# Optimization experiments

Hardware: AMD Instinct MI355X
Metric: run time of the kernel (lower is better)

Reference implementation:

```python
import jax, jax.numpy as jnp
import numpy as np


def setup_inputs() -> dict:
    key = jax.random.key(0)
    kx, kw = jax.random.split(key)
    x = jax.random.normal(kx, (8192, 4096), dtype=jnp.float32)
    # weights initialized ~ N(0, 0.1) as in RandomNormal(stddev=0.1)
    w = jax.random.normal(kw, (4096, 4096), dtype=jnp.float32) * 0.1
    return {"x": x, "w": w}


def reference(x, w):
    # BinaryDense: sign-binarize both activations and weights, then matmul.
    x_bin = jnp.sign(x)  # [N, d_in], values in {-1, 0, +1}
    w_bin = jnp.sign(w)  # [d_in, units]
    return jnp.matmul(x_bin, w_bin)  # [N, units]
```

## Files before the change

### kernel.cpp

```cpp
#include <hip/hip_runtime.h>


#define M_DIM 8192
#define K_DIM 4096
#define N_DIM 4096
#define KB2   (K_DIM / 2)

typedef int   v4i  __attribute__((ext_vector_type(4)));
typedef int   v8i  __attribute__((ext_vector_type(8)));
typedef float v16f __attribute__((ext_vector_type(16)));

typedef __attribute__((address_space(3))) void lds_void_t;
typedef __attribute__((address_space(1))) void g_void_t;

__device__ __forceinline__ unsigned int nib4(float x) {
    return x > 0.0f ? 0x2u : (x < 0.0f ? 0xAu : 0x0u);
}

__global__ __launch_bounds__(256) void pack_x4(const float* __restrict__ in,
                                               unsigned short* __restrict__ out) {
    size_t t = (size_t)blockIdx.x * 256 + threadIdx.x;
    float4 f = ((const float4*)in)[t];
    unsigned int v = nib4(f.x) | (nib4(f.y) << 4) | (nib4(f.z) << 8) | (nib4(f.w) << 12);
    out[t] = (unsigned short)v;
}

__global__ __launch_bounds__(256) void pack_w4(const float* __restrict__ w,
                                               unsigned char* __restrict__ wT) {
    __shared__ unsigned char sT[64][132];
    const int t  = threadIdx.x;
    const int n0 = blockIdx.x * 128;
    const int k0 = blockIdx.y * 64;

    const int cq = t & 31;
    const int r0 = t >> 5;
#pragma unroll
    for (int p = 0; p < 8; ++p) {
        int r = r0 + 8 * p;
        float4 f = *(const float4*)(w + (size_t)(k0 + r) * N_DIM + n0 + cq * 4);
        uchar4 c;
        c.x = (unsigned char)nib4(f.x);
        c.y = (unsigned char)nib4(f.y);
        c.z = (unsigned char)nib4(f.z);
        c.w = (unsigned char)nib4(f.w);
        *(uchar4*)(&sT[r][cq * 4]) = c;
    }
    __syncthreads();

    const int n  = t >> 1;
    const int kq = t & 1;
    union { unsigned char b[16]; int4 v; } u;
#pragma unroll
    for (int j = 0; j < 16; ++j) {
        unsigned lo = sT[kq * 32 + 2 * j][n];
        unsigned hi = sT[kq * 32 + 2 * j + 1][n];
        u.b[j] = (unsigned char)(lo | (hi << 4));
    }
    *(int4*)(wT + (size_t)(n0 + n) * KB2 + (size_t)blockIdx.y * 32 + kq * 16) = u.v;
}

__device__ __forceinline__ v8i widen(v4i x) {
    v8i r;
    r[0] = x[0]; r[1] = x[1]; r[2] = x[2]; r[3] = x[3];
    r[4] = 0; r[5] = 0; r[6] = 0; r[7] = 0;
    return r;
}

__global__ __launch_bounds__(256) void bgemm_fp4(const unsigned char* __restrict__ A,
                                                 const unsigned char* __restrict__ B,
                                                 float* __restrict__ C) {
    __shared__ unsigned char sA[128 * 64];
    __shared__ unsigned char sB[128 * 64];

    const int tid  = threadIdx.x;
    const int lane = tid & 63;
    const int wave = tid >> 6;
    const int wm   = wave >> 1;
    const int wn   = wave & 1;
    const int l31  = lane & 31;
    const int lhi  = lane >> 5;

    const int m0 = blockIdx.y * 128;
    const int n0 = blockIdx.x * 128;

    v16f acc[2][2] = {};

    const unsigned char* gA[2];
    const unsigned char* gB[2];
    int ldsOff[2];
#pragma unroll
    for (int i = 0; i < 2; ++i) {
        int g  = tid + i * 256;
        int m  = g >> 2;
        int kc = (g & 3) ^ ((m >> 1) & 3);
        gA[i] = A + (size_t)(m0 + m) * KB2 + kc * 16;
        gB[i] = B + (size_t)(n0 + m) * KB2 + kc * 16;
        ldsOff[i] = g * 16;
    }

    int offA[2][2], offB[2][2];
#pragma unroll
    for (int ks = 0; ks < 2; ++ks) {
#pragma unroll
        for (int tmn = 0; tmn < 2; ++tmn) {
            int mloc = wm * 64 + tmn * 32 + l31;
            int nloc = wn * 64 + tmn * 32 + l31;
            int kcm  = (ks * 2 + lhi) ^ ((mloc >> 1) & 3);
            int kcn  = (ks * 2 + lhi) ^ ((nloc >> 1) & 3);
            offA[ks][tmn] = mloc * 64 + kcm * 16;
            offB[ks][tmn] = nloc * 64 + kcn * 16;
        }
    }

    for (int kt = 0; kt < K_DIM / 128; ++kt) {
        const size_t koff = (size_t)kt * 64;
#pragma unroll
        for (int i = 0; i < 2; ++i) {
            __builtin_amdgcn_global_load_lds((g_void_t*)(gA[i] + koff),
                                             (lds_void_t*)(sA + ldsOff[i]), 16, 0, 0);
            __builtin_amdgcn_global_load_lds((g_void_t*)(gB[i] + koff),
                                             (lds_void_t*)(sB + ldsOff[i]), 16, 0, 0);
        }
        __syncthreads();

#pragma unroll
        for (int ks = 0; ks < 2; ++ks) {
            v4i a4[2], b4[2];
#pragma unroll
            for (int tm = 0; tm < 2; ++tm) a4[tm] = *(const v4i*)(sA + offA[ks][tm]);
#pragma unroll
            for (int tn = 0; tn < 2; ++tn) b4[tn] = *(const v4i*)(sB + offB[ks][tn]);
#pragma unroll
            for (int tm = 0; tm < 2; ++tm)
#pragma unroll
                for (int tn = 0; tn < 2; ++tn)
                    acc[tm][tn] = __builtin_amdgcn_mfma_scale_f32_32x32x64_f8f6f4(
                        widen(a4[tm]), widen(b4[tn]), acc[tm][tn],
                        4, 4,
                        0, 0x7F7F7F7F,
                        0, 0x7F7F7F7F);
        }
        __syncthreads();
    }

#pragma unroll
    for (int tm = 0; tm < 2; ++tm) {
#pragma unroll
        for (int tn = 0; tn < 2; ++tn) {
            const int col  = n0 + wn * 64 + tn * 32 + l31;
            const int rowb = m0 + wm * 64 + tm * 32 + 4 * lhi;
#pragma unroll
            for (int r = 0; r < 16; ++r) {
                int row = rowb + (r & 3) + 8 * (r >> 2);
                C[(size_t)row * N_DIM + col] = acc[tm][tn][r];
            }
        }
    }
}

extern "C" void kernel_launch(void* const* d_in, const int* in_sizes, int n_in,
                              void* d_out, int out_size, void* d_ws, size_t ws_size,
                              hipStream_t stream) {
    const float* x = (const float*)d_in[0];
    const float* w = (const float*)d_in[1];
    float* out = (float*)d_out;

    unsigned char* xq = (unsigned char*)d_ws;
    unsigned char* wq = xq + (size_t)M_DIM * KB2;

    pack_x4<<<dim3(M_DIM * K_DIM / 4 / 256), dim3(256), 0, stream>>>(x, (unsigned short*)xq);
    pack_w4<<<dim3(N_DIM / 128, K_DIM / 64), dim3(256), 0, stream>>>(w, wq);
    bgemm_fp4<<<dim3(N_DIM / 128, M_DIM / 128), dim3(256), 0, stream>>>(xq, wq, out);
}
```

Measured before the change: 328.0 us.

## Double-buffer GEMM LDS via register prefetch, fuse pack kernels, nontemporal stores

Replaces direct global-to-LDS loads with register-staged prefetch into a double-buffered LDS tile, so the next K tile is loaded while MFMAs run on the current one and only one barrier per iteration remains. Merges the two packing kernels into one launch to save launch overhead and let them run concurrently. Output stores become nontemporal to avoid polluting cache. Costs more LDS and registers per block, which may reduce occupancy.

```diff
diff --git a/kernel.cpp b/kernel.cpp
--- a/kernel.cpp
+++ b/kernel.cpp
@@ -5,32 +5,34 @@
 #define K_DIM 4096
 #define N_DIM 4096
 #define KB2   (K_DIM / 2)
+#define NK    (K_DIM / 128)
+#define BUFB  (128 * 64)
 
 typedef int   v4i  __attribute__((ext_vector_type(4)));
 typedef int   v8i  __attribute__((ext_vector_type(8)));
 typedef float v16f __attribute__((ext_vector_type(16)));
 
-typedef __attribute__((address_space(3))) void lds_void_t;
-typedef __attribute__((address_space(1))) void g_void_t;
-
 __device__ __forceinline__ unsigned int nib4(float x) {
     return x > 0.0f ? 0x2u : (x < 0.0f ? 0xAu : 0x0u);
 }
 
-__global__ __launch_bounds__(256) void pack_x4(const float* __restrict__ in,
-                                               unsigned short* __restrict__ out) {
-    size_t t = (size_t)blockIdx.x * 256 + threadIdx.x;
-    float4 f = ((const float4*)in)[t];
-    unsigned int v = nib4(f.x) | (nib4(f.y) << 4) | (nib4(f.z) << 8) | (nib4(f.w) << 12);
-    out[t] = (unsigned short)v;
-}
-
-__global__ __launch_bounds__(256) void pack_w4(const float* __restrict__ w,
-                                               unsigned char* __restrict__ wT) {
+__global__ __launch_bounds__(256) void pack_both(const float* __restrict__ x,
+                                                 unsigned short* __restrict__ xq,
+                                                 const float* __restrict__ w,
+                                                 unsigned char* __restrict__ wT) {
+    if (blockIdx.x < 32768u) {
+        size_t t = (size_t)blockIdx.x * 256 + threadIdx.x;
+        float4 f = ((const float4*)x)[t];
+        unsigned int v = nib4(f.x) | (nib4(f.y) << 4) | (nib4(f.z) << 8) | (nib4(f.w) << 12);
+        xq[t] = (unsigned short)v;
+        return;
+    }
     __shared__ unsigned char sT[64][132];
+    const unsigned id = blockIdx.x - 32768u;
     const int t  = threadIdx.x;
-    const int n0 = blockIdx.x * 128;
-    const int k0 = blockIdx.y * 64;
+    const int n0 = (int)(id & 31) * 128;
+    const int kb = (int)(id >> 5);
+    const int k0 = kb * 64;
 
     const int cq = t & 31;
     const int r0 = t >> 5;
@@ -56,7 +58,7 @@
         unsigned hi = sT[kq * 32 + 2 * j + 1][n];
         u.b[j] = (unsigned char)(lo | (hi << 4));
     }
-    *(int4*)(wT + (size_t)(n0 + n) * KB2 + (size_t)blockIdx.y * 32 + kq * 16) = u.v;
+    *(int4*)(wT + (size_t)(n0 + n) * KB2 + (size_t)kb * 32 + kq * 16) = u.v;
 }
 
 __device__ __forceinline__ v8i widen(v4i x) {
@@ -69,8 +71,8 @@
 __global__ __launch_bounds__(256) void bgemm_fp4(const unsigned char* __restrict__ A,
                                                  const unsigned char* __restrict__ B,
                                                  float* __restrict__ C) {
-    __shared__ unsigned char sA[128 * 64];
-    __shared__ unsigned char sB[128 * 64];
+    __shared__ unsigned char sA[2 * BUFB];
+    __shared__ unsigned char sB[2 * BUFB];
 
     const int tid  = threadIdx.x;
     const int lane = tid & 63;
@@ -112,24 +114,14 @@
         }
     }
 
-    for (int kt = 0; kt < K_DIM / 128; ++kt) {
-        const size_t koff = (size_t)kt * 64;
-#pragma unroll
-        for (int i = 0; i < 2; ++i) {
-            __builtin_amdgcn_global_load_lds((g_void_t*)(gA[i] + koff),
-                                             (lds_void_t*)(sA + ldsOff[i]), 16, 0, 0);
-            __builtin_amdgcn_global_load_lds((g_void_t*)(gB[i] + koff),
-                                             (lds_void_t*)(sB + ldsOff[i]), 16, 0, 0);
-        }
-        __syncthreads();
-
+    auto compute = [&](int bo) {
 #pragma unroll
         for (int ks = 0; ks < 2; ++ks) {
             v4i a4[2], b4[2];
 #pragma unroll
-            for (int tm = 0; tm < 2; ++tm) a4[tm] = *(const v4i*)(sA + offA[ks][tm]);
+            for (int tm = 0; tm < 2; ++tm) a4[tm] = *(const v4i*)(sA + bo + offA[ks][tm]);
 #pragma unroll
-            for (int tn = 0; tn < 2; ++tn) b4[tn] = *(const v4i*)(sB + offB[ks][tn]);
+            for (int tn = 0; tn < 2; ++tn) b4[tn] = *(const v4i*)(sB + bo + offB[ks][tn]);
 #pragma unroll
             for (int tm = 0; tm < 2; ++tm)
 #pragma unroll
@@ -140,8 +132,35 @@
                         0, 0x7F7F7F7F,
                         0, 0x7F7F7F7F);
         }
+    };
+
+    v4i rA[2], rB[2];
+#pragma unroll
+    for (int i = 0; i < 2; ++i) { rA[i] = *(const v4i*)gA[i]; rB[i] = *(const v4i*)gB[i]; }
+#pragma unroll
+    for (int i = 0; i < 2; ++i) {
+        *(v4i*)(sA + ldsOff[i]) = rA[i];
+        *(v4i*)(sB + ldsOff[i]) = rB[i];
+    }
+    __syncthreads();
+
+    for (int kt = 0; kt < NK - 1; ++kt) {
+        const size_t koff = (size_t)(kt + 1) * 64;
+#pragma unroll
+        for (int i = 0; i < 2; ++i) {
+            rA[i] = *(const v4i*)(gA[i] + koff);
+            rB[i] = *(const v4i*)(gB[i] + koff);
+        }
+        compute((kt & 1) * BUFB);
+        const int bn = ((kt + 1) & 1) * BUFB;
+#pragma unroll
+        for (int i = 0; i < 2; ++i) {
+            *(v4i*)(sA + bn + ldsOff[i]) = rA[i];
+            *(v4i*)(sB + bn + ldsOff[i]) = rB[i];
+        }
         __syncthreads();
     }
+    compute(((NK - 1) & 1) * BUFB);
 
 #pragma unroll
     for (int tm = 0; tm < 2; ++tm) {
@@ -152,7 +171,7 @@
 #pragma unroll
             for (int r = 0; r < 16; ++r) {
                 int row = rowb + (r & 3) + 8 * (r >> 2);
-                C[(size_t)row * N_DIM + col] = acc[tm][tn][r];
+                __builtin_nontemporal_store(acc[tm][tn][r], &C[(size_t)row * N_DIM + col]);
             }
         }
     }
@@ -168,7 +187,7 @@
     unsigned char* xq = (unsigned char*)d_ws;
     unsigned char* wq = xq + (size_t)M_DIM * KB2;
 
-    pack_x4<<<dim3(M_DIM * K_DIM / 4 / 256), dim3(256), 0, stream>>>(x, (unsigned short*)xq);
-    pack_w4<<<dim3(N_DIM / 128, K_DIM / 64), dim3(256), 0, stream>>>(w, wq);
+    pack_both<<<dim3(32768 + 2048), dim3(256), 0, stream>>>(
+        x, (unsigned short*)xq, w, wq);
     bgemm_fp4<<<dim3(N_DIM / 128, M_DIM / 128), dim3(256), 0, stream>>>(xq, wq, out);
 }
```

Measured after the change: 326.4 us. About the same (-0.5%).

## Pack operands in MFMA-fragment order and load directly to registers

Applied to the files above, without the earlier changes.

The packing kernels now write the binarized x and w in a layout grouped by 32-row blocks and 16-byte k-chunks, so each wave lane can read its MFMA fragment straight from global memory. The GEMM drops LDS staging and both barriers and instead double-buffers fragments in registers, prefetching the next k-tile while the current one computes. The two pack kernels are merged into one launch, and output stores are marked nontemporal. In exchange there is no LDS reuse across the waves in a block, so each wave issues its own global loads, and register pressure grows.

```diff
diff --git a/kernel.cpp b/kernel.cpp
--- a/kernel.cpp
+++ b/kernel.cpp
@@ -5,32 +5,49 @@
 #define K_DIM 4096
 #define N_DIM 4096
 #define KB2   (K_DIM / 2)
+#define NKG   (KB2 / 16)
+#define GRPB  (NKG * 32 * 16)
+#define NK    (K_DIM / 128)
 
 typedef int   v4i  __attribute__((ext_vector_type(4)));
 typedef int   v8i  __attribute__((ext_vector_type(8)));
 typedef float v16f __attribute__((ext_vector_type(16)));
 
-typedef __attribute__((address_space(3))) void lds_void_t;
-typedef __attribute__((address_space(1))) void g_void_t;
-
 __device__ __forceinline__ unsigned int nib4(float x) {
     return x > 0.0f ? 0x2u : (x < 0.0f ? 0xAu : 0x0u);
 }
 
-__global__ __launch_bounds__(256) void pack_x4(const float* __restrict__ in,
-                                               unsigned short* __restrict__ out) {
-    size_t t = (size_t)blockIdx.x * 256 + threadIdx.x;
-    float4 f = ((const float4*)in)[t];
-    unsigned int v = nib4(f.x) | (nib4(f.y) << 4) | (nib4(f.z) << 8) | (nib4(f.w) << 12);
-    out[t] = (unsigned short)v;
-}
-
-__global__ __launch_bounds__(256) void pack_w4(const float* __restrict__ w,
-                                               unsigned char* __restrict__ wT) {
+__global__ __launch_bounds__(256) void pack_both(const float* __restrict__ x,
+                                                 unsigned char* __restrict__ xq,
+                                                 const float* __restrict__ w,
+                                                 unsigned char* __restrict__ wq) {
+    const int t = threadIdx.x;
+    if (blockIdx.x < 1024u) {
+        const int mg = blockIdx.x >> 2;
+        const int ks = blockIdx.x & 3;
+        const int r  = t & 31;
+        const int kgbase = ks * 32 + (t >> 5) * 4;
+        const float* row = x + (size_t)(mg * 32 + r) * K_DIM;
+        unsigned char* outb = xq + (size_t)mg * GRPB + r * 16;
+#pragma unroll
+        for (int j = 0; j < 4; ++j) {
+            const int kg = kgbase + j;
+            union { unsigned char b[16]; int4 v; } u;
+#pragma unroll
+            for (int i = 0; i < 8; ++i) {
+                float4 f = *(const float4*)(row + kg * 32 + i * 4);
+                u.b[i * 2]     = (unsigned char)(nib4(f.x) | (nib4(f.y) << 4));
+                u.b[i * 2 + 1] = (unsigned char)(nib4(f.z) | (nib4(f.w) << 4));
+            }
+            *(int4*)(outb + (size_t)kg * 512) = u.v;
+        }
+        return;
+    }
     __shared__ unsigned char sT[64][132];
-    const int t  = threadIdx.x;
-    const int n0 = blockIdx.x * 128;
-    const int k0 = blockIdx.y * 64;
+    const unsigned id = blockIdx.x - 1024u;
+    const int n0 = (int)(id & 31) * 128;
+    const int kb = (int)(id >> 5);
+    const int k0 = kb * 64;
 
     const int cq = t & 31;
     const int r0 = t >> 5;
@@ -56,7 +73,10 @@
         unsigned hi = sT[kq * 32 + 2 * j + 1][n];
         u.b[j] = (unsigned char)(lo | (hi << 4));
     }
-    *(int4*)(wT + (size_t)(n0 + n) * KB2 + (size_t)blockIdx.y * 32 + kq * 16) = u.v;
+    const int ng = (n0 >> 5) + (n >> 5);
+    const int kg = kb * 2 + kq;
+    const int rl = n & 31;
+    *(int4*)(wq + (size_t)ng * GRPB + (size_t)kg * 512 + rl * 16) = u.v;
 }
 
 __device__ __forceinline__ v8i widen(v4i x) {
@@ -69,9 +89,6 @@
 __global__ __launch_bounds__(256) void bgemm_fp4(const unsigned char* __restrict__ A,
                                                  const unsigned char* __restrict__ B,
                                                  float* __restrict__ C) {
-    __shared__ unsigned char sA[128 * 64];
-    __shared__ unsigned char sB[128 * 64];
-
     const int tid  = threadIdx.x;
     const int lane = tid & 63;
     const int wave = tid >> 6;
@@ -83,64 +100,47 @@
     const int m0 = blockIdx.y * 128;
     const int n0 = blockIdx.x * 128;
 
+    const unsigned char* pA[2];
+    const unsigned char* pB[2];
+#pragma unroll
+    for (int tm = 0; tm < 2; ++tm)
+        pA[tm] = A + (size_t)((m0 >> 5) + wm * 2 + tm) * GRPB + lane * 16;
+#pragma unroll
+    for (int tn = 0; tn < 2; ++tn)
+        pB[tn] = B + (size_t)((n0 >> 5) + wn * 2 + tn) * GRPB + lane * 16;
+
     v16f acc[2][2] = {};
+    v4i a[2][2][2], b[2][2][2];
 
-    const unsigned char* gA[2];
-    const unsigned char* gB[2];
-    int ldsOff[2];
+    auto loadTile = [&](int buf, int kt) {
+        const int off = kt * 2048;
 #pragma unroll
-    for (int i = 0; i < 2; ++i) {
-        int g  = tid + i * 256;
-        int m  = g >> 2;
-        int kc = (g & 3) ^ ((m >> 1) & 3);
-        gA[i] = A + (size_t)(m0 + m) * KB2 + kc * 16;
-        gB[i] = B + (size_t)(n0 + m) * KB2 + kc * 16;
-        ldsOff[i] = g * 16;
-    }
-
-    int offA[2][2], offB[2][2];
+        for (int ks = 0; ks < 2; ++ks)
 #pragma unroll
-    for (int ks = 0; ks < 2; ++ks) {
+            for (int tt = 0; tt < 2; ++tt) {
+                a[buf][ks][tt] = *(const v4i*)(pA[tt] + off + ks * 1024);
+                b[buf][ks][tt] = *(const v4i*)(pB[tt] + off + ks * 1024);
+            }
+    };
+    auto compute = [&](int buf) {
 #pragma unroll
-        for (int tmn = 0; tmn < 2; ++tmn) {
-            int mloc = wm * 64 + tmn * 32 + l31;
-            int nloc = wn * 64 + tmn * 32 + l31;
-            int kcm  = (ks * 2 + lhi) ^ ((mloc >> 1) & 3);
-            int kcn  = (ks * 2 + lhi) ^ ((nloc >> 1) & 3);
-            offA[ks][tmn] = mloc * 64 + kcm * 16;
-            offB[ks][tmn] = nloc * 64 + kcn * 16;
-        }
-    }
-
-    for (int kt = 0; kt < K_DIM / 128; ++kt) {
-        const size_t koff = (size_t)kt * 64;
-#pragma unroll
-        for (int i = 0; i < 2; ++i) {
-            __builtin_amdgcn_global_load_lds((g_void_t*)(gA[i] + koff),
-                                             (lds_void_t*)(sA + ldsOff[i]), 16, 0, 0);
-            __builtin_amdgcn_global_load_lds((g_void_t*)(gB[i] + koff),
-                                             (lds_void_t*)(sB + ldsOff[i]), 16, 0, 0);
-        }
-        __syncthreads();
-
-#pragma unroll
-        for (int ks = 0; ks < 2; ++ks) {
-            v4i a4[2], b4[2];
-#pragma unroll
-            for (int tm = 0; tm < 2; ++tm) a4[tm] = *(const v4i*)(sA + offA[ks][tm]);
-#pragma unroll
-            for (int tn = 0; tn < 2; ++tn) b4[tn] = *(const v4i*)(sB + offB[ks][tn]);
+        for (int ks = 0; ks < 2; ++ks)
 #pragma unroll
             for (int tm = 0; tm < 2; ++tm)
 #pragma unroll
                 for (int tn = 0; tn < 2; ++tn)
                     acc[tm][tn] = __builtin_amdgcn_mfma_scale_f32_32x32x64_f8f6f4(
-                        widen(a4[tm]), widen(b4[tn]), acc[tm][tn],
+                        widen(a[buf][ks][tm]), widen(b[buf][ks][tn]), acc[tm][tn],
                         4, 4,
                         0, 0x7F7F7F7F,
                         0, 0x7F7F7F7F);
-        }
-        __syncthreads();
+    };
+
+    loadTile(0, 0);
+    for (int kt = 0; kt < NK; ++kt) {
+        const int cur = kt & 1;
+        if (kt + 1 < NK) loadTile(cur ^ 1, kt + 1);
+        compute(cur);
     }
 
 #pragma unroll
@@ -152,7 +152,7 @@
 #pragma unroll
             for (int r = 0; r < 16; ++r) {
                 int row = rowb + (r & 3) + 8 * (r >> 2);
-                C[(size_t)row * N_DIM + col] = acc[tm][tn][r];
+                __builtin_nontemporal_store(acc[tm][tn][r], &C[(size_t)row * N_DIM + col]);
             }
         }
     }
@@ -168,7 +168,6 @@
     unsigned char* xq = (unsigned char*)d_ws;
     unsigned char* wq = xq + (size_t)M_DIM * KB2;
 
-    pack_x4<<<dim3(M_DIM * K_DIM / 4 / 256), dim3(256), 0, stream>>>(x, (unsigned short*)xq);
-    pack_w4<<<dim3(N_DIM / 128, K_DIM / 64), dim3(256), 0, stream>>>(w, wq);
+    pack_both<<<dim3(1024 + 2048), dim3(256), 0, stream>>>(x, xq, w, wq);
     bgemm_fp4<<<dim3(N_DIM / 128, M_DIM / 128), dim3(256), 0, stream>>>(xq, wq, out);
 }
```

After: 340.5 us. 3.8% more time.
